# Optimization experiments

Measured on AMD Instinct MI355X. Metric: run time of the kernel, lower is better.

Reference implementation:

```python
import jax, jax.numpy as jnp
import numpy as np

N = 1_000_000   # total points across all frames in batch
B = 8           # frames (segments) per batch
C = 256         # bottleneck / backbone_out_channels
H = 512         # lstm_hidden_channels
NUM_CLASSES = 20


def setup_inputs() -> dict:
    key = jax.random.key(0)
    ks = jax.random.split(key, 10)
    s = lambda k, shape, scale=0.02: jax.random.normal(k, shape, dtype=jnp.float32) * scale
    feat = jax.random.normal(ks[0], (N, C), dtype=jnp.float32)
    # cumulative offsets: equal-size segments ending at N (torch offset convention)
    offset = (jnp.arange(1, B + 1, dtype=jnp.int32) * (N // B)).astype(jnp.int32)
    return {
        "feat": feat,
        "offset": offset,
        "W_ih": s(ks[1], (4 * H, C)),
        "b_ih": s(ks[2], (4 * H,)),
        "W_hh": s(ks[3], (4 * H, H)),
        "b_hh": s(ks[4], (4 * H,)),
        "W_proj": s(ks[5], (C, H)),
        "b_proj": s(ks[6], (C,)),
        "W_head": s(ks[7], (NUM_CLASSES, C)),
        "b_head": s(ks[8], (NUM_CLASSES,)),
    }


def reference(feat, offset, W_ih, b_ih, W_hh, b_hh, W_proj, b_proj, W_head, b_head):
    n = feat.shape[0]
    # --- ragged per-segment mean pooling (replaces Python loop over offsets) ---
    seg_id = jnp.searchsorted(offset, jnp.arange(n, dtype=offset.dtype), side="right")
    counts = offset - jnp.concatenate([jnp.zeros((1,), offset.dtype), offset[:-1]])
    sums = jax.ops.segment_sum(feat, seg_id, num_segments=offset.shape[0])  # [B, C]
    pooled = sums / counts[:, None].astype(feat.dtype)                      # [B, C]
    # --- LSTMCell with zero initial (h, c): torch gate order i, f, g, o ---
    gates = pooled @ W_ih.T + b_ih + b_hh                                   # h0 = 0 -> W_hh term drops
    i, f, g, o = jnp.split(gates, 4, axis=-1)
    c = jax.nn.sigmoid(i) * jnp.tanh(g)                                     # f * c0 = 0
    h = jax.nn.sigmoid(o) * jnp.tanh(c)                                     # [B, H]
    _ = jax.nn.sigmoid(f)  # f gate unused with zero cell state (kept implicit)
    # --- temporal projection + broadcast fuse (dropout p=0 in eval) ---
    ctx = h @ W_proj.T + b_proj                                             # [B, C]
    fused = feat + ctx[seg_id]                                              # [N, C]
    # --- segmentation head ---
    seg_logits = fused @ W_head.T + b_head                                  # [N, num_classes]
    return seg_logits
```

## Files before the change

### kernel.cpp

```cpp
#include <hip/hip_runtime.h>
#include <math.h>

#define CDIM 256
#define HDIM 512
#define KCLS 20
#define MAXSEG 8
#define TILE_R 64
#define NTHR 512
#define GRIDA 512
#define F4_TILE (TILE_R * CDIM / 4)
#define F4_THR (F4_TILE / NTHR)

#define BARRIER_LDS_ONLY()                                   \
  do {                                                       \
    asm volatile("s_waitcnt lgkmcnt(0)" ::: "memory");       \
    __builtin_amdgcn_s_barrier();                            \
    __builtin_amdgcn_sched_barrier(0);                       \
  } while (0)

__global__ __launch_bounds__(NTHR, 4) void fused_pool_head_kernel(
    const float* __restrict__ feat, const int* __restrict__ offset,
    const float* __restrict__ W_head, const float* __restrict__ b_head,
    float* __restrict__ sums, float* __restrict__ out, int n, int nseg) {
  __shared__ float tile[TILE_R * CDIM];
  float4* tile4 = (float4*)tile;
  int t = threadIdx.x;
  int lane = t & 63;
  int wv = t >> 6;

  int kb_ = (wv < 4) ? wv * 3 : 12 + (wv - 4) * 2;
  int kb = __builtin_amdgcn_readfirstlane(kb_);
  float bh0 = b_head[kb], bh1 = b_head[kb + 1];
  float bh2 = (wv < 4) ? b_head[kb + 2] : 0.f;

  int ntiles = (n + TILE_R - 1) / TILE_R;
  int nb = (int)gridDim.x;
  int t0 = (int)blockIdx.x;

  int off[MAXSEG];
#pragma unroll
  for (int q = 0; q < MAXSEG; ++q) off[q] = (q < nseg) ? offset[q] : 0x7fffffff;

  int col = t & 255;
  int rhalf = (t >> 8) * 32;
  int c4s = col >> 2, js = col & 3;
  float colacc = 0.f;
  int cur_seg = -1;

  const float4* src = (const float4*)feat;
  long lim = (long)n * (CDIM / 4);
  float4 stgA[F4_THR], stgB[F4_THR];

  auto issue = [&](float4* stg, int tl) {
    long base = (long)tl * F4_TILE;
    if (base + F4_TILE <= lim) {
#pragma unroll
      for (int i = 0; i < F4_THR; ++i) stg[i] = src[base + i * NTHR + t];
    } else {
#pragma unroll
      for (int i = 0; i < F4_THR; ++i) {
        long idx = base + i * NTHR + t;
        stg[i] = (idx < lim) ? src[idx] : make_float4(0.f, 0.f, 0.f, 0.f);
      }
    }
  };
  auto dswrite = [&](const float4* stg) {
#pragma unroll
    for (int i = 0; i < F4_THR; ++i) {
      int idx = i * NTHR + t;
      int rr = idx >> 6, c4 = idx & 63;
      tile4[rr * 64 + (c4 ^ (rr & 7))] = stg[i];
    }
  };
  auto compute = [&](int tl) {
    long r0 = (long)tl * TILE_R;
    int rows = (int)(((long)n - r0) < TILE_R ? ((long)n - r0) : TILE_R);

    {
      int rlo = rhalf, rhi = rhalf + 32;
      if (rhi > rows) rhi = rows;
      if (rlo < rhi) {
        long ra = r0 + rlo, rb = r0 + rhi - 1;
        int s0 = 0, s1 = 0;
#pragma unroll
        for (int q = 0; q < MAXSEG - 1; ++q) {
          s0 += (ra >= off[q]) ? 1 : 0;
          s1 += (rb >= off[q]) ? 1 : 0;
        }
        if (s0 == s1) {
          if (s0 != cur_seg) {
            if (cur_seg >= 0) atomicAdd(&sums[cur_seg * CDIM + col], colacc);
            colacc = 0.f;
            cur_seg = s0;
          }
          float a = 0.f;
#pragma unroll 8
          for (int rr = rlo; rr < rhi; ++rr)
            a += tile[(rr * 64 + (c4s ^ (rr & 7))) * 4 + js];
          colacc += a;
        } else {
          for (int rr = rlo; rr < rhi; ++rr) {
            long r = r0 + rr;
            int s = 0;
#pragma unroll
            for (int q = 0; q < MAXSEG - 1; ++q) s += (r >= off[q]) ? 1 : 0;
            if (s != cur_seg) {
              if (cur_seg >= 0) atomicAdd(&sums[cur_seg * CDIM + col], colacc);
              colacc = 0.f;
              cur_seg = s;
            }
            colacc += tile[(rr * 64 + (c4s ^ (rr & 7))) * 4 + js];
          }
        }
      }
    }

    if (lane < rows) {
      const float4* trow = tile4 + lane * 64;
      int l7 = lane & 7;
      if (wv < 4) {
        float a0 = bh0, a1 = bh1, a2 = bh2;
        const float* w0 = W_head + (size_t)(kb + 0) * CDIM;
        const float* w1 = W_head + (size_t)(kb + 1) * CDIM;
        const float* w2 = W_head + (size_t)(kb + 2) * CDIM;
#pragma unroll 4
        for (int c4 = 0; c4 < 64; ++c4) {
          float4 f = trow[c4 ^ l7];
          int cb = c4 * 4;
          a0 = fmaf(f.x, w0[cb], a0);   a1 = fmaf(f.x, w1[cb], a1);   a2 = fmaf(f.x, w2[cb], a2);
          a0 = fmaf(f.y, w0[cb+1], a0); a1 = fmaf(f.y, w1[cb+1], a1); a2 = fmaf(f.y, w2[cb+1], a2);
          a0 = fmaf(f.z, w0[cb+2], a0); a1 = fmaf(f.z, w1[cb+2], a1); a2 = fmaf(f.z, w2[cb+2], a2);
          a0 = fmaf(f.w, w0[cb+3], a0); a1 = fmaf(f.w, w1[cb+3], a1); a2 = fmaf(f.w, w2[cb+3], a2);
        }
        float* orow = out + (r0 + lane) * KCLS + kb;
        orow[0] = a0; orow[1] = a1; orow[2] = a2;
      } else {
        float a0 = bh0, a1 = bh1;
        const float* w0 = W_head + (size_t)(kb + 0) * CDIM;
        const float* w1 = W_head + (size_t)(kb + 1) * CDIM;
#pragma unroll 4
        for (int c4 = 0; c4 < 64; ++c4) {
          float4 f = trow[c4 ^ l7];
          int cb = c4 * 4;
          a0 = fmaf(f.x, w0[cb], a0);   a1 = fmaf(f.x, w1[cb], a1);
          a0 = fmaf(f.y, w0[cb+1], a0); a1 = fmaf(f.y, w1[cb+1], a1);
          a0 = fmaf(f.z, w0[cb+2], a0); a1 = fmaf(f.z, w1[cb+2], a1);
          a0 = fmaf(f.w, w0[cb+3], a0); a1 = fmaf(f.w, w1[cb+3], a1);
        }
        float* orow = out + (r0 + lane) * KCLS + kb;
        orow[0] = a0; orow[1] = a1;
      }
    }
  };

  if (t0 < ntiles) {
    issue(stgA, t0);
    issue(stgB, t0 + nb < ntiles ? t0 + nb : t0);
    dswrite(stgA);
    BARRIER_LDS_ONLY();

    for (int tl = t0; tl < ntiles; tl += 2 * nb) {
      int tA2 = tl + 2 * nb;
      if (tA2 < ntiles) issue(stgA, tA2);
      compute(tl);
      BARRIER_LDS_ONLY();
      int tB = tl + nb;
      if (tB < ntiles) {
        dswrite(stgB);
        BARRIER_LDS_ONLY();
        int tB2 = tl + 3 * nb;
        if (tB2 < ntiles) issue(stgB, tB2);
        compute(tB);
        BARRIER_LDS_ONLY();
        if (tA2 < ntiles) {
          dswrite(stgA);
          BARRIER_LDS_ONLY();
        }
      }
    }
    if (cur_seg >= 0) atomicAdd(&sums[cur_seg * CDIM + col], colacc);
  }
}

__global__ __launch_bounds__(256) void lstm_h_kernel(
    const float* __restrict__ sums, const int* __restrict__ offset,
    const float* __restrict__ W_ih, const float* __restrict__ b_ih,
    const float* __restrict__ b_hh, float* __restrict__ h, int nseg) {
  __shared__ float pooled[MAXSEG * CDIM];
  int t = threadIdx.x;
  {
    int prev = 0;
    for (int s = 0; s < MAXSEG; ++s) {
      int cur = (s < nseg) ? offset[s] : prev;
      float cnt = (float)(cur - prev);
      float inv = (cnt > 0.f) ? 1.f / cnt : 0.f;
      pooled[s * CDIM + t] = sums[s * CDIM + t] * inv;
      prev = cur;
    }
  }
  __syncthreads();

  int wv = t >> 6, l = t & 63;
  int j = (int)blockIdx.x * 4 + wv;
  int s = l >> 3, ch = l & 7;

  const float4* Wi4 = (const float4*)(W_ih + (size_t)(0 * HDIM + j) * CDIM);
  const float4* Wg4 = (const float4*)(W_ih + (size_t)(2 * HDIM + j) * CDIM);
  const float4* Wo4 = (const float4*)(W_ih + (size_t)(3 * HDIM + j) * CDIM);
  const float4* p4 = (const float4*)(pooled + s * CDIM);

  float di = 0.f, dg = 0.f, dd = 0.f;
#pragma unroll
  for (int i = 0; i < 8; ++i) {
    int c4 = ch * 8 + i;
    float4 p = p4[c4];
    float4 wi = Wi4[c4], wg = Wg4[c4], wo = Wo4[c4];
    di = fmaf(p.x, wi.x, di); di = fmaf(p.y, wi.y, di);
    di = fmaf(p.z, wi.z, di); di = fmaf(p.w, wi.w, di);
    dg = fmaf(p.x, wg.x, dg); dg = fmaf(p.y, wg.y, dg);
    dg = fmaf(p.z, wg.z, dg); dg = fmaf(p.w, wg.w, dg);
    dd = fmaf(p.x, wo.x, dd); dd = fmaf(p.y, wo.y, dd);
    dd = fmaf(p.z, wo.z, dd); dd = fmaf(p.w, wo.w, dd);
  }
#pragma unroll
  for (int m = 1; m < 8; m <<= 1) {
    di += __shfl_xor(di, m);
    dg += __shfl_xor(dg, m);
    dd += __shfl_xor(dd, m);
  }
  if (ch == 0 && s < nseg) {
    di += b_ih[j] + b_hh[j];
    dg += b_ih[2 * HDIM + j] + b_hh[2 * HDIM + j];
    dd += b_ih[3 * HDIM + j] + b_hh[3 * HDIM + j];
    float ig = 1.f / (1.f + expf(-di));
    float gg = tanhf(dg);
    float og = 1.f / (1.f + expf(-dd));
    h[(size_t)s * HDIM + j] = og * tanhf(ig * gg);
  }
}

__global__ __launch_bounds__(256) void ctx_kernel(
    const float* __restrict__ h, const float* __restrict__ W_proj,
    const float* __restrict__ b_proj, float* __restrict__ ctx, int nseg) {
  __shared__ float hs[MAXSEG * HDIM];
  int t = threadIdx.x;
  {
    const float4* hsrc = (const float4*)h;
    float4* hdst = (float4*)hs;
#pragma unroll
    for (int i = 0; i < 4; ++i) hdst[i * 256 + t] = hsrc[i * 256 + t];
  }
  __syncthreads();

  int wv = t >> 6, l = t & 63;
  int col = (int)blockIdx.x * 4 + wv;
  int s = l >> 3, ch = l & 7;

  const float4* Wp4 = (const float4*)(W_proj + (size_t)col * HDIM);
  const float4* h4 = (const float4*)(hs + s * HDIM);
  float acc = 0.f;
#pragma unroll
  for (int i = 0; i < 16; ++i) {
    int j4 = ch * 16 + i;
    float4 hv = h4[j4];
    float4 w = Wp4[j4];
    acc = fmaf(hv.x, w.x, acc); acc = fmaf(hv.y, w.y, acc);
    acc = fmaf(hv.z, w.z, acc); acc = fmaf(hv.w, w.w, acc);
  }
#pragma unroll
  for (int m = 1; m < 8; m <<= 1) acc += __shfl_xor(acc, m);
  if (ch == 0 && s < nseg) ctx[s * CDIM + col] = acc + b_proj[col];
}

__global__ __launch_bounds__(256) void delta_kernel(
    const float* __restrict__ ctx, const float* __restrict__ W_head,
    float* __restrict__ delta, int nseg) {
  __shared__ float cs[MAXSEG * CDIM];
  int t = threadIdx.x;
  {
    const float4* csrc = (const float4*)ctx;
    float4* cdst = (float4*)cs;
#pragma unroll
    for (int i = 0; i < 2; ++i) cdst[i * 256 + t] = csrc[i * 256 + t];
  }
  __syncthreads();

  int wv = t >> 6, l = t & 63;
  int k = (int)blockIdx.x * 4 + wv;
  if (k >= KCLS) return;
  int s = l >> 3, ch = l & 7;

  const float4* Wh4 = (const float4*)(W_head + (size_t)k * CDIM);
  const float4* c4 = (const float4*)(cs + s * CDIM);
  float acc = 0.f;
#pragma unroll
  for (int i = 0; i < 8; ++i) {
    int idx = ch * 8 + i;
    float4 cv = c4[idx];
    float4 w = Wh4[idx];
    acc = fmaf(cv.x, w.x, acc); acc = fmaf(cv.y, w.y, acc);
    acc = fmaf(cv.z, w.z, acc); acc = fmaf(cv.w, w.w, acc);
  }
#pragma unroll
  for (int m = 1; m < 8; m <<= 1) acc += __shfl_xor(acc, m);
  if (ch == 0 && s < nseg) delta[s * KCLS + k] = acc;
}

__global__ __launch_bounds__(256) void add_delta_kernel(
    float* __restrict__ out, const int* __restrict__ offset,
    const float* __restrict__ delta, int n, int nseg) {
  __shared__ float dl[MAXSEG * KCLS];
  int t = threadIdx.x;
  if (t < MAXSEG * KCLS) dl[t] = (t < nseg * KCLS) ? delta[t] : 0.f;
  __syncthreads();

  int off[MAXSEG];
#pragma unroll
  for (int q = 0; q < MAXSEG; ++q) off[q] = (q < nseg) ? offset[q] : 0x7fffffff;

  long tot = (long)n * (KCLS / 4);
  long stride = (long)gridDim.x * 256;
  for (long e4 = (long)blockIdx.x * 256 + t; e4 < tot; e4 += stride) {
    long row = e4 / 5;
    int k0 = (int)(e4 - row * 5) * 4;
    int s = 0;
#pragma unroll
    for (int q = 0; q < MAXSEG - 1; ++q) s += (row >= off[q]) ? 1 : 0;
    float4 v = ((float4*)out)[e4];
    const float* d = &dl[s * KCLS + k0];
    v.x += d[0]; v.y += d[1]; v.z += d[2]; v.w += d[3];
    ((float4*)out)[e4] = v;
  }
}

extern "C" void kernel_launch(void* const* d_in, const int* in_sizes, int n_in,
                              void* d_out, int out_size, void* d_ws, size_t ws_size,
                              hipStream_t stream) {
  const float* feat   = (const float*)d_in[0];
  const int*   offset = (const int*)d_in[1];
  const float* W_ih   = (const float*)d_in[2];
  const float* b_ih   = (const float*)d_in[3];
  const float* b_hh   = (const float*)d_in[5];
  const float* W_proj = (const float*)d_in[6];
  const float* b_proj = (const float*)d_in[7];
  const float* W_head = (const float*)d_in[8];
  const float* b_head = (const float*)d_in[9];
  float* out = (float*)d_out;

  int n = in_sizes[0] / CDIM;
  int nseg = in_sizes[1];
  if (nseg > MAXSEG) nseg = MAXSEG;

  float* ws    = (float*)d_ws;
  float* sums  = ws;
  float* h     = ws + MAXSEG * CDIM;
  float* ctx   = ws + MAXSEG * CDIM + MAXSEG * HDIM;
  float* delta = ctx + MAXSEG * CDIM;

  hipMemsetAsync(sums, 0, MAXSEG * CDIM * sizeof(float), stream);
  fused_pool_head_kernel<<<GRIDA, NTHR, 0, stream>>>(feat, offset, W_head, b_head,
                                                     sums, out, n, nseg);
  lstm_h_kernel<<<128, 256, 0, stream>>>(sums, offset, W_ih, b_ih, b_hh, h, nseg);
  ctx_kernel<<<64, 256, 0, stream>>>(h, W_proj, b_proj, ctx, nseg);
  delta_kernel<<<5, 256, 0, stream>>>(ctx, W_head, delta, nseg);
  add_delta_kernel<<<2560, 256, 0, stream>>>(out, offset, delta, n, nseg);
}
```

Baseline: 370.6 us.

## Specialize waves: four compute head logits, four do vectorized column pooling

Waves are now split by role. Waves 0-3 each compute 5 of the 20 head classes for the 64 tile rows. Waves 4-7 each sum 16 rows of the tile using float4 LDS reads, so pooling work is taken off the head-matmul waves. Before, every wave did both a scalar column-sum over 32 rows and a 2-3 class dot product. The change reduces per-wave LDS traffic and branch divergence, but adds load imbalance between the two roles and four atomics per flush instead of one.

```diff
diff --git a/kernel.cpp b/kernel.cpp
--- a/kernel.cpp
+++ b/kernel.cpp
@@ -28,10 +28,9 @@
   int lane = t & 63;
   int wv = t >> 6;
 
-  int kb_ = (wv < 4) ? wv * 3 : 12 + (wv - 4) * 2;
-  int kb = __builtin_amdgcn_readfirstlane(kb_);
-  float bh0 = b_head[kb], bh1 = b_head[kb + 1];
-  float bh2 = (wv < 4) ? b_head[kb + 2] : 0.f;
+  int kb = __builtin_amdgcn_readfirstlane((wv & 3) * 5);
+  float bh0 = b_head[kb + 0], bh1 = b_head[kb + 1], bh2 = b_head[kb + 2];
+  float bh3 = b_head[kb + 3], bh4 = b_head[kb + 4];
 
   int ntiles = (n + TILE_R - 1) / TILE_R;
   int nb = (int)gridDim.x;
@@ -41,15 +40,24 @@
 #pragma unroll
   for (int q = 0; q < MAXSEG; ++q) off[q] = (q < nseg) ? offset[q] : 0x7fffffff;
 
-  int col = t & 255;
-  int rhalf = (t >> 8) * 32;
-  int c4s = col >> 2, js = col & 3;
-  float colacc = 0.f;
+  int rg = wv - 4;
+  float4 colacc = make_float4(0.f, 0.f, 0.f, 0.f);
   int cur_seg = -1;
 
   const float4* src = (const float4*)feat;
   long lim = (long)n * (CDIM / 4);
   float4 stgA[F4_THR], stgB[F4_THR];
+
+  auto flush = [&]() {
+    if (cur_seg >= 0) {
+      float* d = &sums[cur_seg * CDIM + lane * 4];
+      atomicAdd(d + 0, colacc.x);
+      atomicAdd(d + 1, colacc.y);
+      atomicAdd(d + 2, colacc.z);
+      atomicAdd(d + 3, colacc.w);
+      colacc = make_float4(0.f, 0.f, 0.f, 0.f);
+    }
+  };
 
   auto issue = [&](float4* stg, int tl) {
     long base = (long)tl * F4_TILE;
@@ -72,12 +80,13 @@
       tile4[rr * 64 + (c4 ^ (rr & 7))] = stg[i];
     }
   };
+
   auto compute = [&](int tl) {
     long r0 = (long)tl * TILE_R;
     int rows = (int)(((long)n - r0) < TILE_R ? ((long)n - r0) : TILE_R);
 
-    {
-      int rlo = rhalf, rhi = rhalf + 32;
+    if (wv >= 4) {
+      int rlo = rg * 16, rhi = rlo + 16;
       if (rhi > rows) rhi = rows;
       if (rlo < rhi) {
         long ra = r0 + rlo, rb = r0 + rhi - 1;
@@ -88,68 +97,54 @@
           s1 += (rb >= off[q]) ? 1 : 0;
         }
         if (s0 == s1) {
-          if (s0 != cur_seg) {
-            if (cur_seg >= 0) atomicAdd(&sums[cur_seg * CDIM + col], colacc);
-            colacc = 0.f;
-            cur_seg = s0;
+          if (s0 != cur_seg) { flush(); cur_seg = s0; }
+          float4 a = make_float4(0.f, 0.f, 0.f, 0.f);
+#pragma unroll
+          for (int rr = rlo; rr < rhi; ++rr) {
+            float4 v = tile4[rr * 64 + (lane ^ (rr & 7))];
+            a.x += v.x; a.y += v.y; a.z += v.z; a.w += v.w;
           }
-          float a = 0.f;
-#pragma unroll 8
-          for (int rr = rlo; rr < rhi; ++rr)
-            a += tile[(rr * 64 + (c4s ^ (rr & 7))) * 4 + js];
-          colacc += a;
+          colacc.x += a.x; colacc.y += a.y; colacc.z += a.z; colacc.w += a.w;
         } else {
           for (int rr = rlo; rr < rhi; ++rr) {
             long r = r0 + rr;
             int s = 0;
 #pragma unroll
             for (int q = 0; q < MAXSEG - 1; ++q) s += (r >= off[q]) ? 1 : 0;
-            if (s != cur_seg) {
-              if (cur_seg >= 0) atomicAdd(&sums[cur_seg * CDIM + col], colacc);
-              colacc = 0.f;
-              cur_seg = s;
-            }
-            colacc += tile[(rr * 64 + (c4s ^ (rr & 7))) * 4 + js];
+            if (s != cur_seg) { flush(); cur_seg = s; }
+            float4 v = tile4[rr * 64 + (lane ^ (rr & 7))];
+            colacc.x += v.x; colacc.y += v.y; colacc.z += v.z; colacc.w += v.w;
           }
         }
       }
-    }
-
-    if (lane < rows) {
+    } else if (lane < rows) {
       const float4* trow = tile4 + lane * 64;
       int l7 = lane & 7;
-      if (wv < 4) {
-        float a0 = bh0, a1 = bh1, a2 = bh2;
-        const float* w0 = W_head + (size_t)(kb + 0) * CDIM;
-        const float* w1 = W_head + (size_t)(kb + 1) * CDIM;
-        const float* w2 = W_head + (size_t)(kb + 2) * CDIM;
+      float a0 = bh0, a1 = bh1, a2 = bh2, a3 = bh3, a4 = bh4;
+      const float* w0 = W_head + (size_t)(kb + 0) * CDIM;
+      const float* w1 = W_head + (size_t)(kb + 1) * CDIM;
+      const float* w2 = W_head + (size_t)(kb + 2) * CDIM;
+      const float* w3 = W_head + (size_t)(kb + 3) * CDIM;
+      const float* w4 = W_head + (size_t)(kb + 4) * CDIM;
 #pragma unroll 4
-        for (int c4 = 0; c4 < 64; ++c4) {
-          float4 f = trow[c4 ^ l7];
-          int cb = c4 * 4;
-          a0 = fmaf(f.x, w0[cb], a0);   a1 = fmaf(f.x, w1[cb], a1);   a2 = fmaf(f.x, w2[cb], a2);
-          a0 = fmaf(f.y, w0[cb+1], a0); a1 = fmaf(f.y, w1[cb+1], a1); a2 = fmaf(f.y, w2[cb+1], a2);
-          a0 = fmaf(f.z, w0[cb+2], a0); a1 = fmaf(f.z, w1[cb+2], a1); a2 = fmaf(f.z, w2[cb+2], a2);
-          a0 = fmaf(f.w, w0[cb+3], a0); a1 = fmaf(f.w, w1[cb+3], a1); a2 = fmaf(f.w, w2[cb+3], a2);
-        }
-        float* orow = out + (r0 + lane) * KCLS + kb;
-        orow[0] = a0; orow[1] = a1; orow[2] = a2;
-      } else {
-        float a0 = bh0, a1 = bh1;
-        const float* w0 = W_head + (size_t)(kb + 0) * CDIM;
-        const float* w1 = W_head + (size_t)(kb + 1) * CDIM;
-#pragma unroll 4
-        for (int c4 = 0; c4 < 64; ++c4) {
-          float4 f = trow[c4 ^ l7];
-          int cb = c4 * 4;
-          a0 = fmaf(f.x, w0[cb], a0);   a1 = fmaf(f.x, w1[cb], a1);
-          a0 = fmaf(f.y, w0[cb+1], a0); a1 = fmaf(f.y, w1[cb+1], a1);
-          a0 = fmaf(f.z, w0[cb+2], a0); a1 = fmaf(f.z, w1[cb+2], a1);
-          a0 = fmaf(f.w, w0[cb+3], a0); a1 = fmaf(f.w, w1[cb+3], a1);
-        }
-        float* orow = out + (r0 + lane) * KCLS + kb;
-        orow[0] = a0; orow[1] = a1;
+      for (int c4 = 0; c4 < 64; ++c4) {
+        float4 f = trow[c4 ^ l7];
+        int cb = c4 * 4;
+        a0 = fmaf(f.x, w0[cb], a0);   a1 = fmaf(f.x, w1[cb], a1);
+        a2 = fmaf(f.x, w2[cb], a2);   a3 = fmaf(f.x, w3[cb], a3);
+        a4 = fmaf(f.x, w4[cb], a4);
+        a0 = fmaf(f.y, w0[cb+1], a0); a1 = fmaf(f.y, w1[cb+1], a1);
+        a2 = fmaf(f.y, w2[cb+1], a2); a3 = fmaf(f.y, w3[cb+1], a3);
+        a4 = fmaf(f.y, w4[cb+1], a4);
+        a0 = fmaf(f.z, w0[cb+2], a0); a1 = fmaf(f.z, w1[cb+2], a1);
+        a2 = fmaf(f.z, w2[cb+2], a2); a3 = fmaf(f.z, w3[cb+2], a3);
+        a4 = fmaf(f.z, w4[cb+2], a4);
+        a0 = fmaf(f.w, w0[cb+3], a0); a1 = fmaf(f.w, w1[cb+3], a1);
+        a2 = fmaf(f.w, w2[cb+3], a2); a3 = fmaf(f.w, w3[cb+3], a3);
+        a4 = fmaf(f.w, w4[cb+3], a4);
       }
+      float* orow = out + (r0 + lane) * KCLS + kb;
+      orow[0] = a0; orow[1] = a1; orow[2] = a2; orow[3] = a3; orow[4] = a4;
     }
   };
 
@@ -178,7 +173,7 @@
         }
       }
     }
-    if (cur_seg >= 0) atomicAdd(&sums[cur_seg * CDIM + col], colacc);
+    if (wv >= 4) flush();
   }
 }
 
```

After: 788.2 us. 2.13x slower.
